# Kernel optimization log

Hardware: AMD Instinct MI355X
Metric: run time of the kernel (lower is better)

## Reference

```python
import jax, jax.numpy as jnp
import numpy as np

B, S, D, H = 16, 1024, 512, 8
DH = D // H


def setup_inputs() -> dict:
    key = jax.random.key(0)
    ks = jax.random.split(key, 8)
    q = jax.random.normal(ks[0], (B, S, D), dtype=jnp.float32)
    k = jax.random.normal(ks[1], (B, S, D), dtype=jnp.float32)
    v = jax.random.normal(ks[2], (B, S, D), dtype=jnp.float32)
    # causal lower-triangular mask (1 = attend), broadcastable [1,1,S,S]
    mask = jnp.tril(jnp.ones((S, S), dtype=jnp.int32))[None, None]
    # xavier-uniform weights, zero biases (matches _reset_parameters)
    def xavier(rk, fan):
        lim = float(np.sqrt(6.0 / (fan + fan)))
        return jax.random.uniform(rk, (fan, fan), jnp.float32, -lim, lim)
    Wk = xavier(ks[3], D)
    Wv = xavier(ks[4], D)
    Wo = xavier(ks[5], D)
    bk = jnp.zeros((D,), jnp.float32)
    bv = jnp.zeros((D,), jnp.float32)
    bo = jnp.zeros((D,), jnp.float32)
    return {"q": q, "k": k, "v": v, "mask": mask,
            "Wk": Wk, "bk": bk, "Wv": Wv, "bv": bv, "Wo": Wo, "bo": bo,
            "zero_pad": 1}


def reference(q, k, v, mask, Wk, bk, Wv, bv, Wo, bo, zero_pad):
    # key_query_same=True: q and k both use key_linear
    def split_heads(x):  # [B,S,D] -> [B,H,S,DH]
        return x.reshape(B, S, H, DH).transpose(0, 2, 1, 3)

    qh = split_heads(q @ Wk.T + bk)
    kh = split_heads(k @ Wk.T + bk)
    vh = split_heads(v @ Wv.T + bv)

    scores = jnp.einsum('bhqd,bhkd->bhqk', qh, kh) / jnp.sqrt(jnp.float32(DH))
    scores = jnp.where(mask == 0, jnp.float32(-1e32), scores)
    attn = jax.nn.softmax(scores, axis=-1)
    if zero_pad:  # zero out attention of the first query position (simpleKT trick)
        attn = attn.at[:, :, 0, :].set(0.0)
    # dropout p=0.0 (eval) -> identity
    out = jnp.einsum('bhqk,bhkd->bhqd', attn, vh)  # [B,H,S,DH]
    concat = out.transpose(0, 2, 1, 3).reshape(B, S, D)
    return concat @ Wo.T + bo
```

## Files before the change

### kernel.cpp

```cpp
#include <hip/hip_runtime.h>
#include <hip/hip_bf16.h>
#include <math.h>


typedef __attribute__((ext_vector_type(4))) float f32x4;
typedef __attribute__((ext_vector_type(8))) short bf16x8;

__device__ __forceinline__ short f2bf(float f) {
    union { float f; unsigned u; } x; x.f = f;
    unsigned r = x.u + 0x7fffu + ((x.u >> 16) & 1u);
    return (short)(r >> 16);
}
__device__ __forceinline__ short bfscale(short s, float f) {
    union { float f; unsigned u; } x; x.u = ((unsigned)(unsigned short)s) << 16;
    return f2bf(x.f * f);
}

__device__ __forceinline__ void gload_lds16(const void* g, void* l) {
    __builtin_amdgcn_global_load_lds(
        (const __attribute__((address_space(1))) unsigned int*)g,
        (__attribute__((address_space(3))) unsigned int*)l, 16, 0, 0);
}

__global__ void cvt_w_kernel(const float* __restrict__ w0, const float* __restrict__ w1,
                             const float* __restrict__ w2,
                             short* __restrict__ o0, short* __restrict__ o1,
                             short* __restrict__ o2)
{
    int z = blockIdx.y;
    const float* src = z == 0 ? w0 : (z == 1 ? w1 : w2);
    short* dst = z == 0 ? o0 : (z == 1 ? o1 : o2);
    int i = (blockIdx.x * 256 + threadIdx.x) * 4;
    float4 f = *(const float4*)(src + i);
    short4 s;
    s.x = f2bf(f.x); s.y = f2bf(f.y); s.z = f2bf(f.z); s.w = f2bf(f.w);
    *(short4*)(dst + i) = s;
}

template<int IN_BF16, int SPLIT>
__device__ __forceinline__ void gemm_body(const void* __restrict__ Xv,
                                          const short* __restrict__ W,
                                          const float* __restrict__ bias,
                                          void* __restrict__ Out,
                                          int m0, int n0)
{
    constexpr int ASTR = IN_BF16 ? 64 : 72;
    __shared__ short As[128 * ASTR];
    __shared__ short Bs[128 * 64];
    int tid = threadIdx.x;
    int lane = tid & 63, w = tid >> 6;
    int wr = (w >> 1) * 64, wc = (w & 1) * 64;
    int fr = lane & 15, hi = lane >> 4;
    int lrow = lane >> 3;
    int gcol = ((lane & 7) ^ (lrow & 3)) * 8;
    int xsw = ((hi ^ (lane & 3)) * 8);
    f32x4 acc[4][4] = {};

    const float* Xf = (const float*)Xv;
    const short* Xb = (const short*)Xv;

    float4 pf[8];
    if (!IN_BF16) {
        #pragma unroll
        for (int p = 0; p < 8; ++p) {
            int e = (p * 256 + tid) * 4;
            pf[p] = *(const float4*)(Xf + (size_t)(m0 + (e >> 6)) * 512 + (e & 63));
        }
    }

    for (int k0 = 0; k0 < 512; k0 += 64) {
        __syncthreads();
        #pragma unroll
        for (int c = 0; c < 4; ++c) {
            int chunk = w * 4 + c;
            gload_lds16(W + (size_t)(n0 + chunk * 8 + lrow) * 512 + k0 + gcol,
                        &Bs[chunk * 512]);
        }
        if (IN_BF16) {
            #pragma unroll
            for (int c = 0; c < 4; ++c) {
                int chunk = w * 4 + c;
                gload_lds16(Xb + (size_t)(m0 + chunk * 8 + lrow) * 512 + k0 + gcol,
                            &As[chunk * 512]);
            }
        } else {
            #pragma unroll
            for (int p = 0; p < 8; ++p) {
                int e = (p * 256 + tid) * 4;
                short4 s;
                s.x = f2bf(pf[p].x); s.y = f2bf(pf[p].y);
                s.z = f2bf(pf[p].z); s.w = f2bf(pf[p].w);
                *(short4*)&As[(e >> 6) * ASTR + (e & 63)] = s;
            }
        }
        __syncthreads();
        if (!IN_BF16 && k0 + 64 < 512) {
            #pragma unroll
            for (int p = 0; p < 8; ++p) {
                int e = (p * 256 + tid) * 4;
                pf[p] = *(const float4*)(Xf + (size_t)(m0 + (e >> 6)) * 512 + k0 + 64 + (e & 63));
            }
        }
        #pragma unroll
        for (int ks = 0; ks < 2; ++ks) {
            bf16x8 a[4], b[4];
            #pragma unroll
            for (int i = 0; i < 4; ++i) {
                int row = wr + i * 16 + fr;
                a[i] = IN_BF16
                    ? *(const bf16x8*)&As[row * ASTR + ks * 32 + xsw]
                    : *(const bf16x8*)&As[row * ASTR + ks * 32 + hi * 8];
            }
            #pragma unroll
            for (int j = 0; j < 4; ++j)
                b[j] = *(const bf16x8*)&Bs[(wc + j * 16 + fr) * 64 + ks * 32 + xsw];
            #pragma unroll
            for (int i = 0; i < 4; ++i)
                #pragma unroll
                for (int j = 0; j < 4; ++j)
                    acc[i][j] = __builtin_amdgcn_mfma_f32_16x16x32_bf16(a[i], b[j], acc[i][j], 0, 0, 0);
        }
    }
    int row4 = (lane >> 4) * 4;
    #pragma unroll
    for (int i = 0; i < 4; ++i) {
        #pragma unroll
        for (int j = 0; j < 4; ++j) {
            int gn = n0 + wc + j * 16 + fr;
            float bb = bias[gn];
            #pragma unroll
            for (int r = 0; r < 4; ++r) {
                int gm = m0 + wr + i * 16 + row4 + r;
                float v = acc[i][j][r] + bb;
                if (SPLIT == 1) {
                    int bidx = gm >> 10, s = gm & 1023, hh = gn >> 6, dh = gn & 63;
                    ((short*)Out)[((((size_t)bidx * 8 + hh) * 1024) + s) * 64 + dh] = f2bf(v);
                } else if (SPLIT == 2) {
                    int bidx = gm >> 10, s = gm & 1023, hh = gn >> 6, dh = gn & 63;
                    ((short*)Out)[((((size_t)bidx * 8 + hh) * 64) + dh) * 1024 + s] = f2bf(v);
                } else {
                    ((float*)Out)[(size_t)gm * 512 + gn] = v;
                }
            }
        }
    }
}

__global__ __launch_bounds__(256, 3) void proj_qk_kernel(
    const float* __restrict__ q, const float* __restrict__ k,
    const short* __restrict__ wk, const float* __restrict__ bk,
    short* __restrict__ qh, short* __restrict__ kh)
{
    int d = blockIdx.x;
    int wg = (d & 7) * 128 + (d >> 3);
    int z = wg >> 9;
    int rem = wg & 511;
    gemm_body<0, 1>(z ? (const void*)k : (const void*)q, wk, bk,
                    z ? (void*)kh : (void*)qh,
                    (rem >> 2) * 128, (rem & 3) * 128);
}

__global__ __launch_bounds__(256, 3) void proj_v_kernel(
    const float* __restrict__ v, const short* __restrict__ wv,
    const float* __restrict__ bv, short* __restrict__ vh)
{
    int d = blockIdx.x;
    int wg = (d & 7) * 64 + (d >> 3);
    gemm_body<0, 2>(v, wv, bv, vh, (wg >> 2) * 128, (wg & 3) * 128);
}

__global__ __launch_bounds__(256, 3) void proj_o_kernel(
    const short* __restrict__ ob, const short* __restrict__ wo,
    const float* __restrict__ bo, float* __restrict__ out)
{
    int d = blockIdx.x;
    int wg = (d & 7) * 64 + (d >> 3);
    gemm_body<1, 0>(ob, wo, bo, out, (wg >> 2) * 128, (wg & 3) * 128);
}

__global__ __launch_bounds__(256, 4) void attn_kernel(
    const short* __restrict__ QH, const short* __restrict__ KH,
    const short* __restrict__ VT, short* __restrict__ O,
    const int* __restrict__ zp)
{
    __shared__ short Ks[64][72];
    __shared__ short Vt[64][72];
    __shared__ short Ps[4][16][76];
    int tid = threadIdx.x, lane = tid & 63, w = tid >> 6;
    int fr = lane & 15, hi = lane >> 4;
    int d = blockIdx.x;
    int bh = (d & 7) * 16 + ((d >> 3) & 15);
    int qtp = d >> 7;
    const size_t basebh = (size_t)bh << 16;
    const short* Kb = KH + basebh;
    const short* Vb = VT + basebh;
    int r0 = tid >> 3, c0 = (tid & 7) * 8;
    int zero = zp[0];
    int b = bh >> 3, h = bh & 7;
    const float csc = 0.125f * 1.44269504f;

    for (int which = 0; which < 2; ++which) {
        int qt = which ? 15 - qtp : qtp;
        int qrow0 = qt * 64 + w * 16;

        bf16x8 aQ[2];
        {
            const short* qp = QH + basebh + (size_t)(qrow0 + fr) * 64 + hi * 8;
            bf16x8 q0 = *(const bf16x8*)qp;
            bf16x8 q1 = *(const bf16x8*)(qp + 32);
            #pragma unroll
            for (int j = 0; j < 8; ++j) {
                aQ[0][j] = bfscale(q0[j], csc);
                aQ[1][j] = bfscale(q1[j], csc);
            }
        }

        f32x4 oacc[4] = {};
        float lsum[4] = {0.f, 0.f, 0.f, 0.f};

        bf16x8 kA, kB, vA, vB;
        kA = *(const bf16x8*)(Kb + r0 * 64 + c0);
        kB = *(const bf16x8*)(Kb + (r0 + 32) * 64 + c0);
        vA = *(const bf16x8*)(Vb + (size_t)r0 * 1024 + c0);
        vB = *(const bf16x8*)(Vb + (size_t)(r0 + 32) * 1024 + c0);

        for (int kt = 0; kt <= qt; ++kt) {
            __syncthreads();
            *(bf16x8*)&Ks[r0][c0] = kA;
            *(bf16x8*)&Ks[r0 + 32][c0] = kB;
            *(bf16x8*)&Vt[r0][c0] = vA;
            *(bf16x8*)&Vt[r0 + 32][c0] = vB;
            __syncthreads();
            if (kt < qt) {
                const short* kp = Kb + (kt + 1) * 4096;
                const short* vp = Vb + (kt + 1) * 64;
                kA = *(const bf16x8*)(kp + r0 * 64 + c0);
                kB = *(const bf16x8*)(kp + (r0 + 32) * 64 + c0);
                vA = *(const bf16x8*)(vp + (size_t)r0 * 1024 + c0);
                vB = *(const bf16x8*)(vp + (size_t)(r0 + 32) * 1024 + c0);
            }

            f32x4 sa[4] = {};
            #pragma unroll
            for (int kf = 0; kf < 4; ++kf)
                #pragma unroll
                for (int ks = 0; ks < 2; ++ks) {
                    bf16x8 kb = *(const bf16x8*)&Ks[kf * 16 + fr][ks * 32 + hi * 8];
                    sa[kf] = __builtin_amdgcn_mfma_f32_16x16x32_bf16(aQ[ks], kb, sa[kf], 0, 0, 0);
                }

            if (kt == qt) {
                #pragma unroll
                for (int kf = 0; kf < 4; ++kf) {
                    int gk = kt * 64 + kf * 16 + fr;
                    #pragma unroll
                    for (int r = 0; r < 4; ++r) {
                        float p = exp2f(sa[kf][r]);
                        if (gk > qrow0 + hi * 4 + r) p = 0.f;
                        lsum[r] += p;
                        union { float f; unsigned u; } c; c.f = p;
                        Ps[w][hi * 4 + r][kf * 16 + fr] = (short)(c.u >> 16);
                    }
                }
            } else {
                #pragma unroll
                for (int kf = 0; kf < 4; ++kf)
                    #pragma unroll
                    for (int r = 0; r < 4; ++r) {
                        float p = exp2f(sa[kf][r]);
                        lsum[r] += p;
                        union { float f; unsigned u; } c; c.f = p;
                        Ps[w][hi * 4 + r][kf * 16 + fr] = (short)(c.u >> 16);
                    }
            }

            bf16x8 pa[2];
            pa[0] = *(const bf16x8*)&Ps[w][fr][hi * 8];
            pa[1] = *(const bf16x8*)&Ps[w][fr][32 + hi * 8];
            #pragma unroll
            for (int df = 0; df < 4; ++df)
                #pragma unroll
                for (int ks = 0; ks < 2; ++ks) {
                    bf16x8 vb = *(const bf16x8*)&Vt[df * 16 + fr][ks * 32 + hi * 8];
                    oacc[df] = __builtin_amdgcn_mfma_f32_16x16x32_bf16(pa[ks], vb, oacc[df], 0, 0, 0);
                }
        }

        float inv[4];
        #pragma unroll
        for (int r = 0; r < 4; ++r) {
            float rs = lsum[r];
            #pragma unroll
            for (int off = 1; off < 16; off <<= 1) rs += __shfl_xor(rs, off);
            inv[r] = 1.0f / rs;
        }
        #pragma unroll
        for (int df = 0; df < 4; ++df)
            #pragma unroll
            for (int r = 0; r < 4; ++r) {
                int gq = qrow0 + hi * 4 + r;
                float v = oacc[df][r] * inv[r];
                if (zero && gq == 0) v = 0.f;
                O[((size_t)(b * 1024 + gq)) * 512 + h * 64 + df * 16 + fr] = f2bf(v);
            }
    }
}

extern "C" void kernel_launch(void* const* d_in, const int* in_sizes, int n_in,
                              void* d_out, int out_size, void* d_ws, size_t ws_size,
                              hipStream_t stream)
{
    const float* q  = (const float*)d_in[0];
    const float* k  = (const float*)d_in[1];
    const float* v  = (const float*)d_in[2];
    const float* Wk = (const float*)d_in[4];
    const float* bk = (const float*)d_in[5];
    const float* Wv = (const float*)d_in[6];
    const float* bv = (const float*)d_in[7];
    const float* Wo = (const float*)d_in[8];
    const float* bo = (const float*)d_in[9];
    const int*   zp = (const int*)d_in[10];
    float* out = (float*)d_out;

    short* wkb = (short*)d_ws;
    short* wvb = wkb + 262144;
    short* wob = wvb + 262144;
    short* qh  = wob + 262144;
    short* kh  = qh + 8388608;
    short* vh  = kh + 8388608;
    short* ob  = vh + 8388608;

    cvt_w_kernel<<<dim3(256, 3, 1), 256, 0, stream>>>(Wk, Wv, Wo, wkb, wvb, wob);
    proj_qk_kernel<<<dim3(1024, 1, 1), 256, 0, stream>>>(q, k, wkb, bk, qh, kh);
    proj_v_kernel<<<dim3(512, 1, 1), 256, 0, stream>>>(v, wvb, bv, vh);
    attn_kernel<<<dim3(1024, 1, 1), 256, 0, stream>>>(qh, kh, vh, ob, zp);
    proj_o_kernel<<<dim3(512, 1, 1), 256, 0, stream>>>(ob, wob, bo, out);
}
```

Measured before the change: 119.1 us.

## Double-buffer K/V tiles in LDS for attention with one barrier per iteration

The attention kernel now keeps two LDS buffers each for K and V. The next tile is written into the idle buffer while the current one is consumed, and the global prefetch runs two tiles ahead. This cuts the two __syncthreads per key tile down to one and aims to overlap LDS stores with the MFMA work. The cost is more LDS per block, so the launch-bounds occupancy hint drops from 4 to 3. Row padding also changes from 72 to 68 shorts, which leaves 16-byte vector LDS reads misaligned and may change bank-conflict behaviour.

```diff
diff --git a/kernel.cpp b/kernel.cpp
--- a/kernel.cpp
+++ b/kernel.cpp
@@ -178,13 +178,13 @@
     gemm_body<1, 0>(ob, wo, bo, out, (wg >> 2) * 128, (wg & 3) * 128);
 }
 
-__global__ __launch_bounds__(256, 4) void attn_kernel(
+__global__ __launch_bounds__(256, 3) void attn_kernel(
     const short* __restrict__ QH, const short* __restrict__ KH,
     const short* __restrict__ VT, short* __restrict__ O,
     const int* __restrict__ zp)
 {
-    __shared__ short Ks[64][72];
-    __shared__ short Vt[64][72];
+    __shared__ short Ks[2][64][68];
+    __shared__ short Vt[2][64][68];
     __shared__ short Ps[4][16][76];
     int tid = threadIdx.x, lane = tid & 63, w = tid >> 6;
     int fr = lane & 15, hi = lane >> 4;
@@ -223,21 +223,35 @@
         kB = *(const bf16x8*)(Kb + (r0 + 32) * 64 + c0);
         vA = *(const bf16x8*)(Vb + (size_t)r0 * 1024 + c0);
         vB = *(const bf16x8*)(Vb + (size_t)(r0 + 32) * 1024 + c0);
+        *(bf16x8*)&Ks[0][r0][c0] = kA;
+        *(bf16x8*)&Ks[0][r0 + 32][c0] = kB;
+        *(bf16x8*)&Vt[0][r0][c0] = vA;
+        *(bf16x8*)&Vt[0][r0 + 32][c0] = vB;
+        if (qt > 0) {
+            const short* kp = Kb + 4096;
+            const short* vp = Vb + 64;
+            kA = *(const bf16x8*)(kp + r0 * 64 + c0);
+            kB = *(const bf16x8*)(kp + (r0 + 32) * 64 + c0);
+            vA = *(const bf16x8*)(vp + (size_t)r0 * 1024 + c0);
+            vB = *(const bf16x8*)(vp + (size_t)(r0 + 32) * 1024 + c0);
+        }
+        __syncthreads();
 
         for (int kt = 0; kt <= qt; ++kt) {
-            __syncthreads();
-            *(bf16x8*)&Ks[r0][c0] = kA;
-            *(bf16x8*)&Ks[r0 + 32][c0] = kB;
-            *(bf16x8*)&Vt[r0][c0] = vA;
-            *(bf16x8*)&Vt[r0 + 32][c0] = vB;
-            __syncthreads();
+            int cur = kt & 1;
             if (kt < qt) {
-                const short* kp = Kb + (kt + 1) * 4096;
-                const short* vp = Vb + (kt + 1) * 64;
-                kA = *(const bf16x8*)(kp + r0 * 64 + c0);
-                kB = *(const bf16x8*)(kp + (r0 + 32) * 64 + c0);
-                vA = *(const bf16x8*)(vp + (size_t)r0 * 1024 + c0);
-                vB = *(const bf16x8*)(vp + (size_t)(r0 + 32) * 1024 + c0);
+                *(bf16x8*)&Ks[cur ^ 1][r0][c0] = kA;
+                *(bf16x8*)&Ks[cur ^ 1][r0 + 32][c0] = kB;
+                *(bf16x8*)&Vt[cur ^ 1][r0][c0] = vA;
+                *(bf16x8*)&Vt[cur ^ 1][r0 + 32][c0] = vB;
+                if (kt + 1 < qt) {
+                    const short* kp = Kb + (kt + 2) * 4096;
+                    const short* vp = Vb + (kt + 2) * 64;
+                    kA = *(const bf16x8*)(kp + r0 * 64 + c0);
+                    kB = *(const bf16x8*)(kp + (r0 + 32) * 64 + c0);
+                    vA = *(const bf16x8*)(vp + (size_t)r0 * 1024 + c0);
+                    vB = *(const bf16x8*)(vp + (size_t)(r0 + 32) * 1024 + c0);
+                }
             }
 
             f32x4 sa[4] = {};
@@ -245,7 +259,7 @@
             for (int kf = 0; kf < 4; ++kf)
                 #pragma unroll
                 for (int ks = 0; ks < 2; ++ks) {
-                    bf16x8 kb = *(const bf16x8*)&Ks[kf * 16 + fr][ks * 32 + hi * 8];
+                    bf16x8 kb = *(const bf16x8*)&Ks[cur][kf * 16 + fr][ks * 32 + hi * 8];
                     sa[kf] = __builtin_amdgcn_mfma_f32_16x16x32_bf16(aQ[ks], kb, sa[kf], 0, 0, 0);
                 }
 
@@ -281,9 +295,10 @@
             for (int df = 0; df < 4; ++df)
                 #pragma unroll
                 for (int ks = 0; ks < 2; ++ks) {
-                    bf16x8 vb = *(const bf16x8*)&Vt[df * 16 + fr][ks * 32 + hi * 8];
+                    bf16x8 vb = *(const bf16x8*)&Vt[cur][df * 16 + fr][ks * 32 + hi * 8];
                     oacc[df] = __builtin_amdgcn_mfma_f32_16x16x32_bf16(pa[ks], vb, oacc[df], 0, 0, 0);
                 }
+            __syncthreads();
         }
 
         float inv[4];
```

Result: no change. 118.8 us (-0.3%).

## Enlarge attention query tile to 128 rows with 8 waves per block

Applied to the files above, without the earlier changes.

The attention kernel now uses 512-thread blocks of 8 waves, each block covering a 128-row query tile, and the grid is halved. Each K/V tile loaded into LDS is shared by twice as many query rows, which cuts global K/V traffic and staging work per query. Waves whose rows lie entirely before a key tile skip its compute but still take part in the barriers. This adds idle causal work inside a block and lowers occupancy to two blocks per CU.

```diff
diff --git a/kernel.cpp b/kernel.cpp
--- a/kernel.cpp
+++ b/kernel.cpp
@@ -178,19 +178,19 @@
     gemm_body<1, 0>(ob, wo, bo, out, (wg >> 2) * 128, (wg & 3) * 128);
 }
 
-__global__ __launch_bounds__(256, 4) void attn_kernel(
+__global__ __launch_bounds__(512, 2) void attn_kernel(
     const short* __restrict__ QH, const short* __restrict__ KH,
     const short* __restrict__ VT, short* __restrict__ O,
     const int* __restrict__ zp)
 {
     __shared__ short Ks[64][72];
     __shared__ short Vt[64][72];
-    __shared__ short Ps[4][16][76];
+    __shared__ short Ps[8][16][76];
     int tid = threadIdx.x, lane = tid & 63, w = tid >> 6;
     int fr = lane & 15, hi = lane >> 4;
     int d = blockIdx.x;
     int bh = (d & 7) * 16 + ((d >> 3) & 15);
-    int qtp = d >> 7;
+    int p = d >> 7;
     const size_t basebh = (size_t)bh << 16;
     const short* Kb = KH + basebh;
     const short* Vb = VT + basebh;
@@ -200,8 +200,10 @@
     const float csc = 0.125f * 1.44269504f;
 
     for (int which = 0; which < 2; ++which) {
-        int qt = which ? 15 - qtp : qtp;
-        int qrow0 = qt * 64 + w * 16;
+        int qt = which ? 7 - p : p;
+        int qrow0 = qt * 128 + w * 16;
+        int qtop = qrow0 + 15;
+        int nkt = 2 * qt + 2;
 
         bf16x8 aQ[2];
         {
@@ -218,27 +220,22 @@
         f32x4 oacc[4] = {};
         float lsum[4] = {0.f, 0.f, 0.f, 0.f};
 
-        bf16x8 kA, kB, vA, vB;
+        bf16x8 kA, vA;
         kA = *(const bf16x8*)(Kb + r0 * 64 + c0);
-        kB = *(const bf16x8*)(Kb + (r0 + 32) * 64 + c0);
         vA = *(const bf16x8*)(Vb + (size_t)r0 * 1024 + c0);
-        vB = *(const bf16x8*)(Vb + (size_t)(r0 + 32) * 1024 + c0);
-
-        for (int kt = 0; kt <= qt; ++kt) {
+
+        for (int kt = 0; kt < nkt; ++kt) {
             __syncthreads();
             *(bf16x8*)&Ks[r0][c0] = kA;
-            *(bf16x8*)&Ks[r0 + 32][c0] = kB;
             *(bf16x8*)&Vt[r0][c0] = vA;
-            *(bf16x8*)&Vt[r0 + 32][c0] = vB;
             __syncthreads();
-            if (kt < qt) {
+            if (kt + 1 < nkt) {
                 const short* kp = Kb + (kt + 1) * 4096;
                 const short* vp = Vb + (kt + 1) * 64;
                 kA = *(const bf16x8*)(kp + r0 * 64 + c0);
-                kB = *(const bf16x8*)(kp + (r0 + 32) * 64 + c0);
                 vA = *(const bf16x8*)(vp + (size_t)r0 * 1024 + c0);
-                vB = *(const bf16x8*)(vp + (size_t)(r0 + 32) * 1024 + c0);
-            }
+            }
+            if (kt * 64 > qtop) continue;
 
             f32x4 sa[4] = {};
             #pragma unroll
@@ -249,16 +246,16 @@
                     sa[kf] = __builtin_amdgcn_mfma_f32_16x16x32_bf16(aQ[ks], kb, sa[kf], 0, 0, 0);
                 }
 
-            if (kt == qt) {
+            if (kt * 64 + 63 > qrow0) {
                 #pragma unroll
                 for (int kf = 0; kf < 4; ++kf) {
                     int gk = kt * 64 + kf * 16 + fr;
                     #pragma unroll
                     for (int r = 0; r < 4; ++r) {
-                        float p = exp2f(sa[kf][r]);
-                        if (gk > qrow0 + hi * 4 + r) p = 0.f;
-                        lsum[r] += p;
-                        union { float f; unsigned u; } c; c.f = p;
+                        float pv = exp2f(sa[kf][r]);
+                        if (gk > qrow0 + hi * 4 + r) pv = 0.f;
+                        lsum[r] += pv;
+                        union { float f; unsigned u; } c; c.f = pv;
                         Ps[w][hi * 4 + r][kf * 16 + fr] = (short)(c.u >> 16);
                     }
                 }
@@ -267,9 +264,9 @@
                 for (int kf = 0; kf < 4; ++kf)
                     #pragma unroll
                     for (int r = 0; r < 4; ++r) {
-                        float p = exp2f(sa[kf][r]);
-                        lsum[r] += p;
-                        union { float f; unsigned u; } c; c.f = p;
+                        float pv = exp2f(sa[kf][r]);
+                        lsum[r] += pv;
+                        union { float f; unsigned u; } c; c.f = pv;
                         Ps[w][hi * 4 + r][kf * 16 + fr] = (short)(c.u >> 16);
                     }
             }
@@ -333,6 +330,6 @@
     cvt_w_kernel<<<dim3(256, 3, 1), 256, 0, stream>>>(Wk, Wv, Wo, wkb, wvb, wob);
     proj_qk_kernel<<<dim3(1024, 1, 1), 256, 0, stream>>>(q, k, wkb, bk, qh, kh);
     proj_v_kernel<<<dim3(512, 1, 1), 256, 0, stream>>>(v, wvb, bv, vh);
-    attn_kernel<<<dim3(1024, 1, 1), 256, 0, stream>>>(qh, kh, vh, ob, zp);
+    attn_kernel<<<dim3(512, 1, 1), 512, 0, stream>>>(qh, kh, vh, ob, zp);
     proj_o_kernel<<<dim3(512, 1, 1), 256, 0, stream>>>(ob, wob, bo, out);
 }
```

Result: faster. 114.7 us (-3.7%).
